# Kernel optimization log

Measured on AMD Instinct MI355X. Metric: run time of the kernel, lower is better.

The kernel has to match this reference:

```python
import jax, jax.numpy as jnp
import numpy as np

SIZE_MIN, SIZE_MAX = 10.0, 40.0
CROP = 28


def convert_to_box_list(x):
    # [B, C, W, H] -> [W*H, B, C]
    b, c, w, h = x.shape
    return jnp.transpose(x, (2, 3, 0, 1)).reshape(w * h, b, c)


def invert_convert_to_box_list(x, w, h):
    # [W*H, B, C] -> [B, C, W, H]
    n, b, c = x.shape
    return jnp.transpose(x.reshape(w, h, b, c), (2, 3, 0, 1))


def bilinear_sample(img, x, y):
    # img: [C, W, H]; x, y: pixel coords of shape S -> [C, *S]; zero outside.
    C, W, H = img.shape
    x0 = jnp.floor(x); y0 = jnp.floor(y)
    x1 = x0 + 1.0; y1 = y0 + 1.0
    wx1 = x - x0; wx0 = 1.0 - wx1
    wy1 = y - y0; wy0 = 1.0 - wy1
    def fetch(xi, yi):
        valid = ((xi >= 0) & (xi < W) & (yi >= 0) & (yi < H)).astype(img.dtype)
        xc = jnp.clip(xi, 0, W - 1).astype(jnp.int32)
        yc = jnp.clip(yi, 0, H - 1).astype(jnp.int32)
        return img[:, xc, yc] * valid
    return (fetch(x0, y0) * (wx0 * wy0) + fetch(x1, y0) * (wx1 * wy0)
            + fetch(x0, y1) * (wx0 * wy1) + fetch(x1, y1) * (wx1 * wy1))


def crop(bx, by, bw, bh, big, ws, hs):
    # bx..bh: [k, B]; big: [B, C, W, H] -> [k, B, C, ws, hs]
    u = (jnp.arange(ws) + 0.5) / ws
    v = (jnp.arange(hs) + 0.5) / hs
    xs = bx[..., None] - 0.5 * bw[..., None] + u * bw[..., None] - 0.5  # [k,B,ws]
    ys = by[..., None] - 0.5 * bh[..., None] + v * bh[..., None] - 0.5  # [k,B,hs]
    def one(xr, yr, img):
        X = jnp.broadcast_to(xr[:, None], (ws, hs))
        Y = jnp.broadcast_to(yr[None, :], (ws, hs))
        return bilinear_sample(img, X, Y)
    return jax.vmap(jax.vmap(one, (0, 0, 0)), (0, 0, None))(xs, ys, big)


def uncrop(bx, by, bw, bh, small, Wb, Hb):
    # small: [k, B, C, ws, hs] -> [k, B, C, Wb, Hb] (zero outside each box)
    ws, hs = small.shape[-2], small.shape[-1]
    Xc = jnp.arange(Wb) + 0.5
    Yc = jnp.arange(Hb) + 0.5
    xs = (Xc - (bx[..., None] - 0.5 * bw[..., None])) / bw[..., None] * ws - 0.5
    ys = (Yc - (by[..., None] - 0.5 * bh[..., None])) / bh[..., None] * hs - 0.5
    def one(xr, yr, img):
        X = jnp.broadcast_to(xr[:, None], (Wb, Hb))
        Y = jnp.broadcast_to(yr[None, :], (Wb, Hb))
        return bilinear_sample(img, X, Y)
    return jax.vmap(jax.vmap(one, (0, 0, 0)), (0, 0, 0))(xs, ys, small)


def tmaps_to_bb(tmaps, W_raw, H_raw):
    # tmaps: [B, 4, nw, nh] in (0,1) -> box lists [n_all, B]
    nw, nh = tmaps.shape[-2], tmaps.shape[-1]
    tx, ty, tw, th = tmaps[:, 0], tmaps[:, 1], tmaps[:, 2], tmaps[:, 3]
    ix = jnp.arange(nw, dtype=tmaps.dtype)[:, None]
    iy = jnp.arange(nh, dtype=tmaps.dtype)[None, :]
    bx_map = W_raw * (ix + tx) / nw
    by_map = H_raw * (iy + ty) / nh
    bw_map = SIZE_MIN + (SIZE_MAX - SIZE_MIN) * tw
    bh_map = SIZE_MIN + (SIZE_MAX - SIZE_MIN) * th
    tolist = lambda m: convert_to_box_list(m[:, None]).squeeze(-1)
    return tolist(bx_map), tolist(by_map), tolist(bw_map), tolist(bh_map)


def forward_core(logit_mu, zwhere_mu, zwhere_std, eps_zwhere, eps_zinstance,
                 features, w_zwhere, b_zwhere, w_enc, b_enc, w_dec, b_dec, n_objects_max):
    B, Cf, W_raw, H_raw = features.shape
    nw, nh = logit_mu.shape[-2], logit_mu.shape[-1]

    # zwhere posterior sample + KL vs N(0,1)
    zwhere_sample_map = zwhere_mu + zwhere_std * eps_zwhere
    zwhere_kl_map = 0.5 * (zwhere_mu ** 2 + zwhere_std ** 2) - jnp.log(zwhere_std) - 0.5

    # decode zwhere (1x1 conv) -> sigmoid tmaps -> boxes
    tmaps = jax.nn.sigmoid(jnp.einsum('bzwh,cz->bcwh', zwhere_sample_map, w_zwhere)
                           + b_zwhere[None, :, None, None])
    bx_all, by_all, bw_all, bh_all = tmaps_to_bb(tmaps, W_raw, H_raw)

    area_all = bw_all * bh_all
    area_map = invert_convert_to_box_list(area_all[..., None], nw, nh)

    # c sample = logit map (deterministic relaxation of the DPP/Bernoulli sample)
    c_sample_map = logit_mu
    prob_map = jax.nn.sigmoid(c_sample_map)
    c_all = convert_to_box_list(c_sample_map).squeeze(-1)   # [n_all, B]
    prob_all = convert_to_box_list(prob_map).squeeze(-1)

    # top-k per batch element (indices constant wrt grads)
    k = min(n_objects_max, c_all.shape[0])
    idx = jax.lax.stop_gradient(jax.lax.top_k(c_all.T, k)[1].T)  # [k, B]
    take = lambda t: jnp.take_along_axis(t, idx, axis=0)
    c_few, prob_few = take(c_all), take(prob_all)
    bx_few, by_few, bw_few, bh_few = take(bx_all), take(by_all), take(bw_all), take(bh_all)

    zwhere_sample_all = convert_to_box_list(zwhere_sample_map)  # [n_all, B, Z]
    zwhere_kl_all = convert_to_box_list(zwhere_kl_map)
    idx_z = idx[..., None]
    zwhere_sample_few = jnp.take_along_axis(zwhere_sample_all, idx_z, axis=0)
    zwhere_kl_few = jnp.take_along_axis(zwhere_kl_all, idx_z, axis=0)

    # crop full-res features at the k boxes -> [k, B, Cf, CROP, CROP]
    cropped = crop(bx_few, by_few, bw_few, bh_few, features, CROP, CROP)

    # encoder zinstance (flatten + linear -> mu, std)
    flat = cropped.reshape(k, B, -1)
    enc = jnp.einsum('kbf,df->kbd', flat, w_enc) + b_enc
    dim_z = enc.shape[-1] // 2
    zi_mu = enc[..., :dim_z]
    zi_std = jax.nn.softplus(enc[..., dim_z:]) + 1e-4
    zi_sample = zi_mu + zi_std * eps_zinstance
    zi_kl = 0.5 * (zi_mu ** 2 + zi_std ** 2) - jnp.log(zi_std) - 0.5

    # decoder zinstance (linear -> [k, B, 2, CROP, CROP])
    dec = jnp.einsum('kbz,fz->kbf', zi_sample, w_dec) + b_dec
    raw = dec.reshape(k, B, 2, CROP, CROP)
    small = jnp.concatenate([jax.nn.softplus(raw[..., :1, :, :]),
                             jax.nn.sigmoid(raw[..., 1:, :, :])], axis=-3)

    big_stuff = uncrop(bx_few, by_few, bw_few, bh_few,
                       small * c_few[..., None, None, None], W_raw, H_raw)
    big_weight = big_stuff[..., :1, :, :]
    big_img = big_stuff[..., 1:, :, :]

    # from_weights_to_masks over box dim (dim=-5 of [k,B,1,W,H])
    sum_w = jnp.sum(big_weight, axis=0, keepdims=True)
    big_mask = jnp.tanh(sum_w) * (big_weight / jnp.maximum(sum_w, 1e-6))
    big_mask_non = jnp.tanh(big_weight)

    return (prob_map, area_map, c_few, prob_few, bx_few, by_few, bw_few, bh_few,
            big_mask, big_mask_non, big_img,
            zwhere_sample_few, zwhere_kl_few, zi_sample, zi_kl)


def setup_inputs() -> dict:
    key = jax.random.key(0)
    ks = jax.random.split(key, 9)
    B, NW, NH = 8, 32, 32
    W_RAW = H_RAW = 128
    CF, ZW, ZI, K = 32, 8, 32, 48
    fan_in = CF * CROP * CROP
    return {
        "logit_mu": jax.random.normal(ks[0], (B, 1, NW, NH), jnp.float32),
        "zwhere_mu": 0.5 * jax.random.normal(ks[1], (B, ZW, NW, NH), jnp.float32),
        "zwhere_std": jax.random.uniform(ks[2], (B, ZW, NW, NH), jnp.float32, 0.1, 1.0),
        "eps_zwhere": jax.random.normal(ks[3], (B, ZW, NW, NH), jnp.float32),
        "eps_zinstance": jax.random.normal(ks[4], (K, B, ZI), jnp.float32),
        "features": jax.random.normal(ks[5], (B, CF, W_RAW, H_RAW), jnp.float32),
        "w_zwhere": 0.3 * jax.random.normal(ks[6], (4, ZW), jnp.float32),
        "b_zwhere": jnp.zeros((4,), jnp.float32),
        "w_enc": jax.random.normal(ks[7], (2 * ZI, fan_in), jnp.float32) / np.sqrt(fan_in).astype(np.float32),
        "b_enc": jnp.zeros((2 * ZI,), jnp.float32),
        "w_dec": jax.random.normal(ks[8], (2 * CROP * CROP, ZI), jnp.float32) / np.sqrt(ZI).astype(np.float32),
        "b_dec": jnp.zeros((2 * CROP * CROP,), jnp.float32),
        "n_objects_max": 48,
    }


def reference(logit_mu, zwhere_mu, zwhere_std, eps_zwhere, eps_zinstance, features,
              w_zwhere, b_zwhere, w_enc, b_enc, w_dec, b_dec, n_objects_max):
    return forward_core(logit_mu, zwhere_mu, zwhere_std, eps_zwhere, eps_zinstance,
                        features, w_zwhere, b_zwhere, w_enc, b_enc, w_dec, b_dec,
                        n_objects_max)
```

## Files before the change

### kernel.cpp

```cpp
#include <hip/hip_runtime.h>
#include <math.h>

#define B 8
#define NWD 32
#define NHD 32
#define NBOX 1024
#define ZWD 8
#define ZID 32
#define KOBJ 48
#define CFEAT 32
#define WRAW 128
#define HRAW 128
#define CR 28
#define CR2 784
#define FAN 25088
#define KB 384

#define OFF_PROB   0
#define OFF_AREA   8192
#define OFF_CFEW   16384
#define OFF_PFEW   16768
#define OFF_BXF    17152
#define OFF_BYF    17536
#define OFF_BWF    17920
#define OFF_BHF    18304
#define OFF_BMASK  18688
#define OFF_BMASKN 6310144
#define OFF_BIMG   12601600
#define OFF_ZWS    18893056
#define OFF_ZWK    18896128
#define OFF_ZIS    18899200
#define OFF_ZIK    18911488

#define WS_SMALL 32768

#define SCR_PART 0
#define SCR_WT   2752512

#define FSPLIT 28
#define FPB 896
#define CHK 224
#define NCH 4
#define MKB 16
#define KSTR 232
#define TAPN (MKB*28)

typedef __attribute__((ext_vector_type(8))) short bfrag;
typedef __attribute__((ext_vector_type(4))) float f32x4;

__device__ __forceinline__ float sigm(float x){ return 1.0f/(1.0f+expf(-x)); }
__device__ __forceinline__ float softpl(float x){ return fmaxf(x,0.0f) + log1pf(expf(-fabsf(x))); }
__device__ __forceinline__ float ftanh(float x){
  float t = __expf(2.0f*x);
  return 1.0f - __fdividef(2.0f, t + 1.0f);
}
__device__ __forceinline__ unsigned short f2bf(float f){
  unsigned u = __float_as_uint(f);
  unsigned r = u + 0x7FFFu + ((u >> 16) & 1u);
  return (unsigned short)(r >> 16);
}
__device__ __forceinline__ unsigned okey(float f){
  unsigned b = __float_as_uint(f);
  return b ^ ((b & 0x80000000u) ? 0xFFFFFFFFu : 0x80000000u);
}

__global__ __launch_bounds__(256) void prep_kernel(
    const float* __restrict__ wenc, unsigned short* __restrict__ wt,
    const float* __restrict__ logit, const float* __restrict__ zmu,
    const float* __restrict__ zstd, const float* __restrict__ zeps,
    const float* __restrict__ wz, const float* __restrict__ bz,
    float* __restrict__ out){
  __shared__ __align__(16) unsigned su[NBOX];
  if (blockIdx.x < 784){
    const int gid = blockIdx.x*256 + threadIdx.x;
    const int lane = gid & 63;
    const int rest = gid >> 6;
    const int t = rest & 3;
    const int rest2 = rest >> 2;
    const int s = rest2 % 7;
    const int fsc = rest2 / 7;
    const int d = t*16 + (lane & 15);
    const int k0 = fsc*CHK + s*32 + (lane >> 4)*8;
    const float* src = wenc + (size_t)d*FAN + k0;
    float4 a = *(const float4*)src;
    float4 b = *(const float4*)(src + 4);
    unsigned long long p0 = (unsigned long long)f2bf(a.x)
      | ((unsigned long long)f2bf(a.y) << 16)
      | ((unsigned long long)f2bf(a.z) << 32)
      | ((unsigned long long)f2bf(a.w) << 48);
    unsigned long long p1 = (unsigned long long)f2bf(b.x)
      | ((unsigned long long)f2bf(b.y) << 16)
      | ((unsigned long long)f2bf(b.z) << 32)
      | ((unsigned long long)f2bf(b.w) << 48);
    unsigned short* dst = wt + (size_t)gid*8;
    *(unsigned long long*)dst       = p0;
    *(unsigned long long*)(dst + 4) = p1;
    return;
  }
  const int bid = blockIdx.x - 784;
  const int b  = bid >> 2;
  const int sb = bid & 3;
  const int tid = threadIdx.x;
  #pragma unroll
  for (int u = 0; u < 4; u++){
    int j = tid + u*256;
    su[j] = okey(logit[b*NBOX + j]);
  }
  const int n = sb*256 + tid;
  const int w = n >> 5, h = n & 31;
  float acc0=bz[0], acc1=bz[1], acc2=bz[2], acc3=bz[3];
  #pragma unroll
  for(int z=0; z<ZWD; z++){
    int id = ((b*ZWD + z)*NWD + w)*NHD + h;
    float s = zmu[id] + zstd[id]*zeps[id];
    acc0 += s*wz[0*ZWD+z]; acc1 += s*wz[1*ZWD+z];
    acc2 += s*wz[2*ZWD+z]; acc3 += s*wz[3*ZWD+z];
  }
  float tx=sigm(acc0), ty=sigm(acc1), tw=sigm(acc2), th=sigm(acc3);
  float bx = (128.0f*((float)w + tx))/32.0f;
  float by = (128.0f*((float)h + ty))/32.0f;
  float bwv = 10.0f + 30.0f*tw;
  float bhv = 10.0f + 30.0f*th;
  float lg = logit[b*NBOX + n];
  out[OFF_PROB + b*NBOX + n] = sigm(lg);
  out[OFF_AREA + b*NBOX + n] = bwv*bhv;
  __syncthreads();
  const unsigned ui = su[n];
  const uint4* su4 = (const uint4*)su;
  int rank = 0;
  #pragma unroll 4
  for (int jq = 0; jq < NBOX/4; jq++){
    uint4 v = su4[jq];
    int j = jq*4;
    rank += (v.x > ui || (v.x == ui && j   < n)) ? 1 : 0;
    rank += (v.y > ui || (v.y == ui && j+1 < n)) ? 1 : 0;
    rank += (v.z > ui || (v.z == ui && j+2 < n)) ? 1 : 0;
    rank += (v.w > ui || (v.w == ui && j+3 < n)) ? 1 : 0;
  }
  if (rank < KOBJ){
    out[OFF_CFEW + rank*B + b] = lg;
    out[OFF_PFEW + rank*B + b] = sigm(lg);
    out[OFF_BXF  + rank*B + b] = bx;
    out[OFF_BYF  + rank*B + b] = by;
    out[OFF_BWF  + rank*B + b] = bwv;
    out[OFF_BHF  + rank*B + b] = bhv;
    #pragma unroll
    for(int z=0; z<ZWD; z++){
      int id = ((b*ZWD + z)*NWD + w)*NHD + h;
      float mu = zmu[id], sd = zstd[id];
      out[OFF_ZWS + (rank*B+b)*ZWD + z] = mu + sd*zeps[id];
      out[OFF_ZWK + (rank*B+b)*ZWD + z] = 0.5f*(mu*mu + sd*sd) - logf(sd) - 0.5f;
    }
  }
}

__device__ __forceinline__ void sample_chunk(
    int tid, int fs, int ch, int kb0, const float* __restrict__ feat,
    const float2* wxs, const int2* xos, const float2* wys, const int2* yos,
    unsigned short* cl){
  const int kc0 = fs*FPB + ch*CHK;
  #pragma unroll 2
  for (int u = 0; u < 14; u++){
    int idx = u*256 + tid;
    int rr = idx / CHK, ff = idx - rr*CHK;
    int f = kc0 + ff;
    int c = f / CR2; int p = f - c*CR2;
    int i = p / CR;  int j = p - i*CR;
    const float* img = feat + (size_t)(((kb0+rr) & (B-1))*CFEAT + c)*(WRAW*HRAW);
    float2 wx = wxs[rr*28 + i]; int2 xo = xos[rr*28 + i];
    float2 wy = wys[rr*28 + j]; int2 yo = yos[rr*28 + j];
    float v = (img[xo.x+yo.x]*wy.x + img[xo.x+yo.y]*wy.y)*wx.x
            + (img[xo.y+yo.x]*wy.x + img[xo.y+yo.y]*wy.y)*wx.y;
    cl[rr*KSTR + ff] = f2bf(v);
  }
}

__global__ __launch_bounds__(256, 8) void enc_kernel(
    const float* __restrict__ feat, const unsigned short* __restrict__ wt,
    const float* __restrict__ outc, float* __restrict__ part){
  __shared__ __align__(16) unsigned short cl0[MKB*KSTR];
  __shared__ __align__(16) unsigned short cl1[MKB*KSTR];
  __shared__ float2 wxs[TAPN]; __shared__ int2 xos[TAPN];
  __shared__ float2 wys[TAPN]; __shared__ int2 yos[TAPN];
  __shared__ float rAx[MKB], rSx[MKB], rAy[MKB], rSy[MKB];
  const int tid = threadIdx.x;
  const int fs  = blockIdx.x % FSPLIT;
  const int kb0 = (blockIdx.x / FSPLIT) * MKB;
  if (tid < MKB){
    float bx = outc[OFF_BXF + kb0 + tid];
    float by = outc[OFF_BYF + kb0 + tid];
    float bw = outc[OFF_BWF + kb0 + tid];
    float bh = outc[OFF_BHF + kb0 + tid];
    float sx = bw * (1.0f/(float)CR), sy = bh * (1.0f/(float)CR);
    rSx[tid] = sx; rSy[tid] = sy;
    rAx[tid] = bx - 0.5f*bw + 0.5f*sx - 0.5f;
    rAy[tid] = by - 0.5f*bh + 0.5f*sy - 0.5f;
  }
  __syncthreads();
  #pragma unroll
  for (int it = 0; it < 4; it++){
    int idx = it*256 + tid;
    if (idx < 2*TAPN){
      int isy = idx >= TAPN;
      int q = idx - (isy ? TAPN : 0);
      int rr = q / 28, i = q - rr*28;
      float A = isy ? rAy[rr] : rAx[rr];
      float S = isy ? rSy[rr] : rSx[rr];
      float x = fmaf((float)i, S, A);
      float x0f = floorf(x); int x0 = (int)x0f;
      float w1 = x - x0f, w0 = 1.0f - w1;
      if ((unsigned)x0     >= WRAW) w0 = 0.f;
      if ((unsigned)(x0+1) >= WRAW) w1 = 0.f;
      int c0 = min(max(x0,0),WRAW-1), c1 = min(max(x0+1,0),WRAW-1);
      if (isy){ wys[q] = make_float2(w0,w1); yos[q] = make_int2(c0, c1); }
      else    { wxs[q] = make_float2(w0,w1); xos[q] = make_int2(c0*HRAW, c1*HRAW); }
    }
  }
  __syncthreads();
  const int lane = tid & 63, wv = tid >> 6;
  const int lr = lane & 15, lg = lane >> 4;
  f32x4 acc = {0.f,0.f,0.f,0.f};
  sample_chunk(tid, fs, 0, kb0, feat, wxs, xos, wys, yos, cl0);
  __syncthreads();
  #pragma unroll
  for (int ch = 0; ch < NCH; ch++){
    unsigned short* cur = (ch & 1) ? cl1 : cl0;
    unsigned short* nxt = (ch & 1) ? cl0 : cl1;
    if (ch < NCH-1)
      sample_chunk(tid, fs, ch+1, kb0, feat, wxs, xos, wys, yos, nxt);
    const unsigned short* arow  = &cur[lr*KSTR + lg*8];
    const unsigned short* bbase = wt + (size_t)(fs*NCH + ch)*14336 + wv*512 + lane*8;
    #pragma unroll
    for (int s = 0; s < 7; s++){
      bfrag a = *(const bfrag*)(arow + s*32);
      bfrag b = *(const bfrag*)(bbase + s*2048);
      acc = __builtin_amdgcn_mfma_f32_16x16x32_bf16(a, b, acc, 0, 0, 0);
    }
    __syncthreads();
  }
  float* dst = part + ((size_t)fs*KB + kb0)*64;
  #pragma unroll
  for (int r = 0; r < 4; r++){
    int row = lg*4 + r;
    dst[row*64 + wv*16 + lr] = acc[r];
  }
}

__global__ __launch_bounds__(256) void zi_dec_kernel(
    const float* __restrict__ part, const float* __restrict__ benc,
    const float* __restrict__ ieps, const float* __restrict__ wdec,
    const float* __restrict__ bdec, float* __restrict__ out,
    float* __restrict__ ws){
  int kb = blockIdx.x;
  int d = threadIdx.x & 63, seg = threadIdx.x >> 6;
  float s0=0.f, s1=0.f;
  for (int f = seg; f < FSPLIT; f += 8)
    s0 += part[((size_t)f*KB + kb)*64 + d];
  for (int f = seg+4; f < FSPLIT; f += 8)
    s1 += part[((size_t)f*KB + kb)*64 + d];
  __shared__ float red[4][64];
  __shared__ float zs[ZID];
  __shared__ float cf_s;
  red[seg][d] = s0 + s1;
  __syncthreads();
  if (threadIdx.x < ZID){
    int dd = threadIdx.x;
    float mu = benc[dd]     + red[0][dd]     + red[1][dd]     + red[2][dd]     + red[3][dd];
    float pe = benc[ZID+dd] + red[0][ZID+dd] + red[1][ZID+dd] + red[2][ZID+dd] + red[3][ZID+dd];
    float sd = softpl(pe) + 1e-4f;
    float zsv = mu + sd*ieps[kb*ZID + dd];
    out[OFF_ZIS + kb*ZID + dd] = zsv;
    out[OFF_ZIK + kb*ZID + dd] = 0.5f*(mu*mu + sd*sd) - logf(sd) - 0.5f;
    zs[dd] = zsv;
  }
  if (threadIdx.x == 0) cf_s = out[OFF_CFEW + kb];
  __syncthreads();
  float cf = cf_s;
  for (int f = threadIdx.x; f < 2*CR2; f += 256){
    float a = bdec[f];
    #pragma unroll
    for (int q = 0; q < 8; q++){
      float4 w4 = *(const float4*)&wdec[f*ZID + q*4];
      a = fmaf(zs[q*4+0], w4.x, a);
      a = fmaf(zs[q*4+1], w4.y, a);
      a = fmaf(zs[q*4+2], w4.z, a);
      a = fmaf(zs[q*4+3], w4.w, a);
    }
    float v = (f < CR2) ? softpl(a) : sigm(a);
    ws[WS_SMALL + (size_t)kb*(2*CR2) + f] = v*cf;
  }
}

__global__ __launch_bounds__(256) void uncrop_compose_kernel(
    const float* __restrict__ ws, float* __restrict__ out){
  const int t = blockIdx.x*256 + threadIdx.x;
  const int b = t >> 14, p = t & 16383;
  const int X = p >> 7, Y = p & 127;
  __shared__ float sAx[KOBJ], sSx[KOBJ], sAy[KOBJ], sSy[KOBJ];
  if (threadIdx.x < KOBJ){
    int k = threadIdx.x;
    float bx = out[OFF_BXF + k*B + b], bw = out[OFF_BWF + k*B + b];
    float by = out[OFF_BYF + k*B + b], bh = out[OFF_BHF + k*B + b];
    float ix = __fdividef((float)CR, bw), iy = __fdividef((float)CR, bh);
    sSx[k] = ix; sAx[k] = (0.5f*bw - bx)*ix - 0.5f;
    sSy[k] = iy; sAy[k] = (0.5f*bh - by)*iy - 0.5f;
  }
  __syncthreads();
  const float xc = (float)X + 0.5f, yc = (float)Y + 0.5f;
  float wr[KOBJ];
  float sum = 0.f;
  #pragma unroll
  for (int k = 0; k < KOBJ; k++){
    float x = fmaf(xc, sSx[k], sAx[k]);
    float y = fmaf(yc, sSy[k], sAy[k]);
    const float* sm = ws + WS_SMALL + (size_t)(k*B + b)*(2*CR2);
    float x0f = floorf(x), y0f = floorf(y);
    int x0 = (int)x0f, y0 = (int)y0f;
    float wx1 = x - x0f, wx0 = 1.0f - wx1;
    float wy1 = y - y0f, wy0 = 1.0f - wy1;
    if ((unsigned)x0     >= CR) wx0 = 0.f;
    if ((unsigned)(x0+1) >= CR) wx1 = 0.f;
    if ((unsigned)y0     >= CR) wy0 = 0.f;
    if ((unsigned)(y0+1) >= CR) wy1 = 0.f;
    int x0c = min(max(x0,0),CR-1), x1c = min(max(x0+1,0),CR-1);
    int y0c = min(max(y0,0),CR-1), y1c = min(max(y0+1,0),CR-1);
    const float* r0 = sm + x0c*CR;
    const float* r1 = sm + x1c*CR;
    float v0 = (r0[y0c]*wy0 + r0[y1c]*wy1)*wx0 + (r1[y0c]*wy0 + r1[y1c]*wy1)*wx1;
    const float* q0 = r0 + CR2;
    const float* q1 = r1 + CR2;
    float v1 = (q0[y0c]*wy0 + q0[y1c]*wy1)*wx0 + (q1[y0c]*wy0 + q1[y1c]*wy1)*wx1;
    wr[k] = v0; sum += v0;
    out[OFF_BIMG + (size_t)(k*B + b)*16384 + p] = v1;
  }
  float th = ftanh(sum);
  float inv = 1.0f / fmaxf(sum, 1e-6f);
  #pragma unroll
  for (int k = 0; k < KOBJ; k++){
    size_t o = (size_t)(k*B + b)*16384 + p;
    out[OFF_BMASK  + o] = th * (wr[k] * inv);
    out[OFF_BMASKN + o] = ftanh(wr[k]);
  }
}

extern "C" void kernel_launch(void* const* d_in, const int* in_sizes, int n_in,
                              void* d_out, int out_size, void* d_ws, size_t ws_size,
                              hipStream_t stream) {
  (void)in_sizes; (void)n_in; (void)out_size; (void)ws_size;
  const float* logit = (const float*)d_in[0];
  const float* zmu   = (const float*)d_in[1];
  const float* zstd  = (const float*)d_in[2];
  const float* zeps  = (const float*)d_in[3];
  const float* ieps  = (const float*)d_in[4];
  const float* feat  = (const float*)d_in[5];
  const float* wz    = (const float*)d_in[6];
  const float* bz    = (const float*)d_in[7];
  const float* wenc  = (const float*)d_in[8];
  const float* benc  = (const float*)d_in[9];
  const float* wdec  = (const float*)d_in[10];
  const float* bdec  = (const float*)d_in[11];
  float* out = (float*)d_out;
  float* ws  = (float*)d_ws;
  float* scr = out + OFF_BMASK;
  float* part = scr + SCR_PART;
  unsigned short* wt = (unsigned short*)(scr + SCR_WT);

  prep_kernel         <<<784 + B*4, 256, 0, stream>>>(wenc, wt, logit, zmu, zstd, zeps, wz, bz, out);
  enc_kernel          <<<(KB/MKB)*FSPLIT, 256, 0, stream>>>(feat, wt, out, part);
  zi_dec_kernel       <<<KB, 256, 0, stream>>>(part, benc, ieps, wdec, bdec, out, ws);
  uncrop_compose_kernel<<<(B*WRAW*HRAW)/256, 256, 0, stream>>>(ws, out);
}
```

Baseline: 95.10 us.

## Split encoder K into more slices and overlap feature gathers with MFMA

Raises the feature split from 28 to 49 slices with smaller chunks, so more blocks run and each does less serial work. The bilinear sampling is split into a gather phase that loads raw pixels into registers before the MFMAs and a store phase that blends and writes bf16 after them, so global load latency overlaps the matrix math. Weight fragments are prefetched up front, the weight repack layout is simplified to match, and launch bounds drop to 4 waves per SIMD to make room for the extra registers. The cost is more partial sums for the reduction kernel to add up, plus higher register pressure.

After: 92.46 us. 2.8% less time.

```diff
diff --git a/kernel.cpp b/kernel.cpp
--- a/kernel.cpp
+++ b/kernel.cpp
@@ -37,12 +37,12 @@
 #define SCR_PART 0
 #define SCR_WT   2752512
 
-#define FSPLIT 28
-#define FPB 896
-#define CHK 224
+#define FSPLIT 49
+#define FPB 512
+#define CHK 128
 #define NCH 4
 #define MKB 16
-#define KSTR 232
+#define KSTR 152
 #define TAPN (MKB*28)
 
 typedef __attribute__((ext_vector_type(8))) short bfrag;
@@ -72,15 +72,12 @@
     float* __restrict__ out){
   __shared__ __align__(16) unsigned su[NBOX];
   if (blockIdx.x < 784){
-    const int gid = blockIdx.x*256 + threadIdx.x;
-    const int lane = gid & 63;
-    const int rest = gid >> 6;
-    const int t = rest & 3;
-    const int rest2 = rest >> 2;
-    const int s = rest2 % 7;
-    const int fsc = rest2 / 7;
+    const int ks = blockIdx.x;
+    const int tid = threadIdx.x;
+    const int lane = tid & 63;
+    const int t = tid >> 6;
     const int d = t*16 + (lane & 15);
-    const int k0 = fsc*CHK + s*32 + (lane >> 4)*8;
+    const int k0 = ks*32 + (lane >> 4)*8;
     const float* src = wenc + (size_t)d*FAN + k0;
     float4 a = *(const float4*)src;
     float4 b = *(const float4*)(src + 4);
@@ -92,7 +89,7 @@
       | ((unsigned long long)f2bf(b.y) << 16)
       | ((unsigned long long)f2bf(b.z) << 32)
       | ((unsigned long long)f2bf(b.w) << 48);
-    unsigned short* dst = wt + (size_t)gid*8;
+    unsigned short* dst = wt + ((size_t)ks*256 + tid)*8;
     *(unsigned long long*)dst       = p0;
     *(unsigned long long*)(dst + 4) = p1;
     return;
@@ -154,28 +151,7 @@
   }
 }
 
-__device__ __forceinline__ void sample_chunk(
-    int tid, int fs, int ch, int kb0, const float* __restrict__ feat,
-    const float2* wxs, const int2* xos, const float2* wys, const int2* yos,
-    unsigned short* cl){
-  const int kc0 = fs*FPB + ch*CHK;
-  #pragma unroll 2
-  for (int u = 0; u < 14; u++){
-    int idx = u*256 + tid;
-    int rr = idx / CHK, ff = idx - rr*CHK;
-    int f = kc0 + ff;
-    int c = f / CR2; int p = f - c*CR2;
-    int i = p / CR;  int j = p - i*CR;
-    const float* img = feat + (size_t)(((kb0+rr) & (B-1))*CFEAT + c)*(WRAW*HRAW);
-    float2 wx = wxs[rr*28 + i]; int2 xo = xos[rr*28 + i];
-    float2 wy = wys[rr*28 + j]; int2 yo = yos[rr*28 + j];
-    float v = (img[xo.x+yo.x]*wy.x + img[xo.x+yo.y]*wy.y)*wx.x
-            + (img[xo.y+yo.x]*wy.x + img[xo.y+yo.y]*wy.y)*wx.y;
-    cl[rr*KSTR + ff] = f2bf(v);
-  }
-}
-
-__global__ __launch_bounds__(256, 8) void enc_kernel(
+__global__ __launch_bounds__(256, 4) void enc_kernel(
     const float* __restrict__ feat, const unsigned short* __restrict__ wt,
     const float* __restrict__ outc, float* __restrict__ part){
   __shared__ __align__(16) unsigned short cl0[MKB*KSTR];
@@ -217,25 +193,63 @@
     }
   }
   __syncthreads();
+  float raw[8][4];
+  int ji[8];
+  const int fblk = fs*FPB;
+  #define GATHER(CH) { \
+    _Pragma("unroll") \
+    for (int u = 0; u < 8; u++){ \
+      int idx = u*256 + tid; \
+      int rr = idx >> 7, ff = idx & 127; \
+      int f = fblk + (CH)*CHK + ff; \
+      int c = f / CR2; int p = f - c*CR2; \
+      int i = p / CR;  int j = p - i*CR; \
+      int ii = rr*28 + i, jj = rr*28 + j; \
+      ji[u] = (jj << 16) | ii; \
+      int2 xo = xos[ii]; int2 yo = yos[jj]; \
+      const float* img = feat + (size_t)((rr & (B-1))*CFEAT + c)*(WRAW*HRAW); \
+      raw[u][0] = img[xo.x + yo.x]; \
+      raw[u][1] = img[xo.x + yo.y]; \
+      raw[u][2] = img[xo.y + yo.x]; \
+      raw[u][3] = img[xo.y + yo.y]; \
+    } }
+  #define STORE(DST) { \
+    _Pragma("unroll") \
+    for (int u = 0; u < 8; u++){ \
+      int idx = u*256 + tid; \
+      int rr = idx >> 7, ff = idx & 127; \
+      int ii = ji[u] & 0xffff, jj = ji[u] >> 16; \
+      float2 wx = wxs[ii]; float2 wy = wys[jj]; \
+      float v = (raw[u][0]*wy.x + raw[u][1]*wy.y)*wx.x \
+              + (raw[u][2]*wy.x + raw[u][3]*wy.y)*wx.y; \
+      (DST)[rr*KSTR + ff] = f2bf(v); \
+    } }
+  GATHER(0);
+  STORE(cl0);
+  __syncthreads();
   const int lane = tid & 63, wv = tid >> 6;
   const int lr = lane & 15, lg = lane >> 4;
   f32x4 acc = {0.f,0.f,0.f,0.f};
-  sample_chunk(tid, fs, 0, kb0, feat, wxs, xos, wys, yos, cl0);
-  __syncthreads();
   #pragma unroll
   for (int ch = 0; ch < NCH; ch++){
     unsigned short* cur = (ch & 1) ? cl1 : cl0;
     unsigned short* nxt = (ch & 1) ? cl0 : cl1;
-    if (ch < NCH-1)
-      sample_chunk(tid, fs, ch+1, kb0, feat, wxs, xos, wys, yos, nxt);
-    const unsigned short* arow  = &cur[lr*KSTR + lg*8];
-    const unsigned short* bbase = wt + (size_t)(fs*NCH + ch)*14336 + wv*512 + lane*8;
-    #pragma unroll
-    for (int s = 0; s < 7; s++){
-      bfrag a = *(const bfrag*)(arow + s*32);
-      bfrag b = *(const bfrag*)(bbase + s*2048);
-      acc = __builtin_amdgcn_mfma_f32_16x16x32_bf16(a, b, acc, 0, 0, 0);
-    }
+    const unsigned short* bptr = wt + (size_t)(fs*16 + ch*4)*2048 + wv*512 + lane*8;
+    bfrag b0 = *(const bfrag*)(bptr);
+    bfrag b1 = *(const bfrag*)(bptr + 2048);
+    bfrag b2 = *(const bfrag*)(bptr + 4096);
+    bfrag b3 = *(const bfrag*)(bptr + 6144);
+    if (ch < NCH-1){ GATHER(ch+1); }
+    const unsigned short* arow = &cur[lr*KSTR + lg*8];
+    bfrag a0 = *(const bfrag*)(arow);
+    bfrag a1 = *(const bfrag*)(arow + 32);
+    bfrag a2 = *(const bfrag*)(arow + 64);
+    bfrag a3 = *(const bfrag*)(arow + 96);
+    acc = __builtin_amdgcn_mfma_f32_16x16x32_bf16(a0, b0, acc, 0, 0, 0);
+    acc = __builtin_amdgcn_mfma_f32_16x16x32_bf16(a1, b1, acc, 0, 0, 0);
+    acc = __builtin_amdgcn_mfma_f32_16x16x32_bf16(a2, b2, acc, 0, 0, 0);
+    acc = __builtin_amdgcn_mfma_f32_16x16x32_bf16(a3, b3, acc, 0, 0, 0);
+    if (ch < NCH-1){ STORE(nxt); }
     __syncthreads();
   }
   float* dst = part + ((size_t)fs*KB + kb0)*64;
@@ -244,6 +258,8 @@
     int row = lg*4 + r;
     dst[row*64 + wv*16 + lr] = acc[r];
   }
+  #undef GATHER
+  #undef STORE
 }
 
 __global__ __launch_bounds__(256) void zi_dec_kernel(
```
